# Kernel tuning notes

Hardware: AMD Instinct MI355X
Metric: run time of the kernel (lower is better)

Reference implementation:

```python
import jax, jax.numpy as jnp
import numpy as np

B, L, D, H = 2, 4096, 512, 8
HD = D // H
SCALE = 1.0 / (D / H) ** 0.5


def setup_inputs() -> dict:
    key = jax.random.key(0)
    ks = jax.random.split(key, 12)
    s = 0.02
    inp = {
        "q": jax.random.normal(ks[0], (B, L, D), jnp.float32),
        "k": jax.random.normal(ks[1], (B, L, D), jnp.float32),
        "v": jax.random.normal(ks[2], (B, L, D), jnp.float32),
        # causal mask, True = keep (masked_fill where mask == False)
        "mask": jnp.tril(jnp.ones((L, L), bool))[None, None, :, :],
        "Wq": jax.random.normal(ks[3], (D, D), jnp.float32) * s,
        "bq": jnp.zeros((D,), jnp.float32),
        "Wk": jax.random.normal(ks[4], (D, D), jnp.float32) * s,
        "bk": jnp.zeros((D,), jnp.float32),
        "Wv": jax.random.normal(ks[5], (D, D), jnp.float32) * s,
        "bv": jnp.zeros((D,), jnp.float32),
        "Wo": jax.random.normal(ks[6], (D, D), jnp.float32) * s,
        "bo": jnp.zeros((D,), jnp.float32),
    }
    return inp


def _split_heads(x):
    # [B, L, D] -> [B, H, L, HD]
    b, l, d = x.shape
    return x.reshape(b, l, H, HD).transpose(0, 2, 1, 3)


def reference(q, k, v, mask, Wq, bq, Wk, bk, Wv, bv, Wo, bo):
    # Dropout is inference-mode (identity), matching module.eval().
    qh = _split_heads(q @ Wq.T + bq)          # [B,H,L,HD]
    kh = _split_heads(k @ Wk.T + bk)          # [B,H,L,HD]
    vh = _split_heads(v @ Wv.T + bv)          # [B,H,L,HD]
    scores = jnp.einsum("bhqd,bhkd->bhqk", qh, kh) * SCALE
    scores = jnp.where(mask, scores, -jnp.inf)
    attn = jax.nn.softmax(scores, axis=-1)
    out = jnp.einsum("bhqk,bhkd->bhqd", attn, vh)  # [B,H,L,HD]
    out = out.transpose(0, 2, 1, 3).reshape(q.shape[0], q.shape[1], D)
    return out @ Wo.T + bo
```

## Files before the change

### kernel.cpp

```cpp
#include <hip/hip_runtime.h>

typedef __bf16 bf16;
typedef __bf16 bf16x4 __attribute__((ext_vector_type(4)));
typedef __bf16 bf16x8 __attribute__((ext_vector_type(8)));
typedef float  f32x4  __attribute__((ext_vector_type(4)));
typedef float  f32x16 __attribute__((ext_vector_type(16)));
typedef unsigned int u32x2 __attribute__((ext_vector_type(2)));
typedef unsigned int u32x4 __attribute__((ext_vector_type(4)));

#define NB   2
#define NL   4096
#define ND   512
#define NH   8
#define NHD  64

static __device__ __forceinline__ void g2l16(const bf16* g, bf16* l) {
    __builtin_amdgcn_global_load_lds(
        (const __attribute__((address_space(1))) unsigned int*)g,
        (__attribute__((address_space(3))) unsigned int*)l, 16, 0, 0);
}

__global__ __launch_bounds__(256) void cvt_all(
    const float* __restrict__ q, const float* __restrict__ k, const float* __restrict__ v,
    const float* __restrict__ Wq, const float* __restrict__ Wk,
    const float* __restrict__ Wv, const float* __restrict__ Wo,
    bf16* __restrict__ qb, bf16* __restrict__ kb, bf16* __restrict__ vb,
    bf16* __restrict__ wqb, bf16* __restrict__ wkb,
    bf16* __restrict__ wvb, bf16* __restrict__ wob)
{
    const int z = blockIdx.z;
    const float* src; bf16* dst; int n4;
    switch (z) {
        case 0: src = q;  dst = qb;  n4 = NB * NL * ND / 4; break;
        case 1: src = k;  dst = kb;  n4 = NB * NL * ND / 4; break;
        case 2: src = v;  dst = vb;  n4 = NB * NL * ND / 4; break;
        case 3: src = Wq; dst = wqb; n4 = ND * ND / 4; break;
        case 4: src = Wk; dst = wkb; n4 = ND * ND / 4; break;
        case 5: src = Wv; dst = wvb; n4 = ND * ND / 4; break;
        default: src = Wo; dst = wob; n4 = ND * ND / 4; break;
    }
    for (int i = blockIdx.x * 256 + threadIdx.x; i < n4; i += gridDim.x * 256) {
        const f32x4 a = *(const f32x4*)(src + (size_t)i * 4);
        bf16x4 o;
        #pragma unroll
        for (int j = 0; j < 4; ++j) o[j] = (bf16)a[j];
        *(bf16x4*)(dst + (size_t)i * 4) = o;
    }
}

__global__ __launch_bounds__(256) void proj_qkv(
    const bf16* __restrict__ qb, const bf16* __restrict__ kb, const bf16* __restrict__ vb,
    const bf16* __restrict__ wq, const bf16* __restrict__ wk, const bf16* __restrict__ wv,
    const float* __restrict__ biasq, const float* __restrict__ biask, const float* __restrict__ biasv,
    bf16* __restrict__ qh, bf16* __restrict__ kh, bf16* __restrict__ vt)
{
    const int z = blockIdx.z;
    const bf16* X     = (z == 0) ? qb : (z == 1) ? kb : vb;
    const bf16* W     = (z == 0) ? wq : (z == 1) ? wk : wv;
    const float* bias = (z == 0) ? biasq : (z == 1) ? biask : biasv;

    const int m0 = blockIdx.y * 128;
    const int n0 = blockIdx.x * 128;

    __shared__ bf16 As[2][128 * 32];
    __shared__ bf16 Bs[2][128 * 32];

    const int t    = threadIdx.x;
    const int lane = t & 63;
    const int wm   = (t >> 7) & 1;
    const int wn   = (t >> 6) & 1;
    const int quad = lane >> 4;
    const int l16  = lane & 15;

    auto stage = [&](int k0, int buf) {
        #pragma unroll
        for (int p = 0; p < 2; ++p) {
            const int id = p * 256 + t;
            const int r = id >> 2, s = id & 3;
            const int c = (s ^ (r & 3)) * 8;
            g2l16(X + (size_t)(m0 + r) * ND + k0 + c, As[buf] + id * 8);
            g2l16(W + (size_t)(n0 + r) * ND + k0 + c, Bs[buf] + id * 8);
        }
    };

    f32x4 acc[4][4] = {};
    stage(0, 0);

    for (int it = 0; it < 16; ++it) {
        __syncthreads();
        if (it + 1 < 16) stage((it + 1) * 32, (it + 1) & 1);

        const bf16* as = As[it & 1];
        const bf16* bs = Bs[it & 1];
        bf16x8 aF[4], bF[4];
        #pragma unroll
        for (int i = 0; i < 4; ++i) {
            const int ra = wm * 64 + i * 16 + l16;
            const int rb = wn * 64 + i * 16 + l16;
            aF[i] = *(const bf16x8*)(as + ra * 32 + (quad ^ (ra & 3)) * 8);
            bF[i] = *(const bf16x8*)(bs + rb * 32 + (quad ^ (rb & 3)) * 8);
        }
        #pragma unroll
        for (int mt = 0; mt < 4; ++mt)
            #pragma unroll
            for (int nt = 0; nt < 4; ++nt)
                acc[mt][nt] = __builtin_amdgcn_mfma_f32_16x16x32_bf16(
                    aF[mt], bF[nt], acc[mt][nt], 0, 0, 0);
    }

    const float oscale = (z == 0) ? 0.125f : (z == 1) ? 1.4426950408889634f : 1.0f;
    #pragma unroll
    for (int nt = 0; nt < 4; ++nt) {
        const int col = n0 + wn * 64 + nt * 16 + l16;
        const float bb = bias[col];
        const int h = col >> 6, hd = col & 63;
        #pragma unroll
        for (int mt = 0; mt < 4; ++mt) {
            const int row0 = m0 + wm * 64 + mt * 16 + quad * 4;
            const int b = row0 >> 12;
            const int l = row0 & 4095;
            if (z == 2) {
                bf16x4 val;
                #pragma unroll
                for (int r = 0; r < 4; ++r) val[r] = (bf16)(acc[mt][nt][r] + bb);
                *(bf16x4*)(vt + ((size_t)(b * NH + h) * NHD + hd) * NL + l) = val;
            } else {
                bf16* dst = (z == 0) ? qh : kh;
                #pragma unroll
                for (int r = 0; r < 4; ++r)
                    dst[((size_t)(b * NH + h) * NL + (l + r)) * NHD + hd] =
                        (bf16)((acc[mt][nt][r] + bb) * oscale);
            }
        }
    }
}

__global__ __launch_bounds__(512, 1) void attn(
    const bf16* __restrict__ qh, const bf16* __restrict__ kh,
    const bf16* __restrict__ vt, bf16* __restrict__ ao)
{
    const int bh  = blockIdx.x;
    const int b   = bh >> 3, h = bh & 7;
    const int qtA = blockIdx.y;
    const int qtB = 31 - qtA;
    const int nA  = 2 * qtA + 2;

    __shared__ bf16 smem[65536];

    const int t    = threadIdx.x;
    const int wave = t >> 6;
    const int g    = wave >> 2;
    const int w4   = wave & 3;
    const int lane = t & 63;
    const int l32  = lane & 31;
    const int half = lane >> 5;
    const int sb   = g * 32768;
    const int tg   = t & 255;
    const int qrow_l = w4 * 32 + l32;

    const bf16* Qg = qh + (size_t)bh * NL * NHD;
    const bf16* Kg = kh + (size_t)bh * NL * NHD;
    const bf16* Vg = vt + (size_t)bh * NHD * NL;

    auto kv_of = [&](int jn) -> int {
        return (g == 0) ? jn : ((jn < nA) ? jn : jn - nA + 33);
    };

    auto stage_kv = [&](int k0, int buf) {
        bf16* kd = smem + sb + buf * 8192;
        #pragma unroll
        for (int p = 0; p < 2; ++p) {
            const int id = p * 256 + tg;
            const int r = id >> 3, s = id & 7;
            g2l16(Kg + (size_t)(k0 + r) * NHD + ((s ^ (r & 7)) * 8), kd + id * 8);
            g2l16(Vg + (size_t)r * NL + k0 + ((s ^ (r & 7)) * 8), kd + 4096 + id * 8);
        }
    };

    stage_kv(kv_of(0) * 64, 0);
    stage_kv(kv_of(1) * 64, 1);
    stage_kv(kv_of(2) * 64, 2);

    bf16x8 qf[4];
    {
        const int qt0 = (g == 0) ? qtB : qtA;
        const bf16* Qt = Qg + (size_t)(qt0 * 128 + qrow_l) * NHD;
        #pragma unroll
        for (int c = 0; c < 4; ++c)
            qf[c] = *(const bf16x8*)(Qt + c * 16 + half * 8);
    }

    f32x16 o_acc[2] = {};
    float l_lane = 0.f;

    for (int jj = 0; jj < 33; ++jj) {
        if (jj < 31)       asm volatile("s_waitcnt vmcnt(8)" ::: "memory");
        else if (jj == 31) asm volatile("s_waitcnt vmcnt(4)" ::: "memory");
        else               asm volatile("s_waitcnt vmcnt(0)" ::: "memory");
        __builtin_amdgcn_sched_barrier(0);
        __builtin_amdgcn_s_barrier();
        __builtin_amdgcn_sched_barrier(0);

        if (jj + 3 < 33) stage_kv(kv_of(jj + 3) * 64, (jj + 3) & 3);

        if (g == 1 && jj == nA) {
            const float lt = l_lane + __shfl_xor(l_lane, 32, 64);
            const float rcp = 1.0f / fmaxf(lt, 1e-20f);
            const int row = qtA * 128 + qrow_l;
            #pragma unroll
            for (int mt2 = 0; mt2 < 2; ++mt2)
                #pragma unroll
                for (int rr = 0; rr < 4; ++rr) {
                    const int hd = mt2 * 32 + rr * 8 + half * 4;
                    bf16x4 val;
                    #pragma unroll
                    for (int rb = 0; rb < 4; ++rb)
                        val[rb] = (bf16)(o_acc[mt2][rr * 4 + rb] * rcp);
                    *(bf16x4*)(ao + ((size_t)b * NL + row) * ND + h * NHD + hd) = val;
                }
            o_acc[0] = (f32x16)(0.f); o_acc[1] = (f32x16)(0.f);
            l_lane = 0.f;
            const bf16* Qt = Qg + (size_t)(qtB * 128 + qrow_l) * NHD;
            #pragma unroll
            for (int c = 0; c < 4; ++c)
                qf[c] = *(const bf16x8*)(Qt + c * 16 + half * 8);
        }

        const bool useA  = (g == 1) && (jj < nA);
        const int j_glob = kv_of(jj);
        const int qt_cur = useA ? qtA : qtB;

        const bf16* ks = smem + sb + (jj & 3) * 8192;
        const bf16* vs = ks + 4096;

        f32x16 sacc[2] = {};
        #pragma unroll
        for (int c = 0; c < 4; ++c) {
            #pragma unroll
            for (int mt = 0; mt < 2; ++mt) {
                const int row   = mt * 32 + l32;
                const int chunk = 2 * c + half;
                const bf16x8 kf = *(const bf16x8*)(ks + row * 64 + ((chunk ^ (row & 7)) * 8));
                sacc[mt] = __builtin_amdgcn_mfma_f32_32x32x16_bf16(
                    kf, qf[c], sacc[mt], 0, 0, 0);
            }
        }

        const bool diag = (j_glob >= 2 * qt_cur);
        const int  dq   = j_glob * 64 - qt_cur * 128;
        #pragma unroll
        for (int mt = 0; mt < 2; ++mt) {
            #pragma unroll
            for (int r = 0; r < 16; ++r) {
                const int kv = mt * 32 + (r & 3) + 8 * (r >> 2) + 4 * half;
                float e;
                if (diag && (dq + kv > qrow_l)) e = 0.f;
                else e = __builtin_amdgcn_exp2f(sacc[mt][r]);
                l_lane += e;
                sacc[mt][r] = e;
            }
        }

        #pragma unroll
        for (int c = 0; c < 4; ++c) {
            const int mt = c >> 1;
            const int b0 = (c & 1) * 8;
            unsigned w0, w1, w2, w3;
            asm("v_cvt_pk_bf16_f32 %0, %1, %2" : "=v"(w0)
                : "v"(sacc[mt][b0 + 0]), "v"(sacc[mt][b0 + 1]));
            asm("v_cvt_pk_bf16_f32 %0, %1, %2" : "=v"(w1)
                : "v"(sacc[mt][b0 + 2]), "v"(sacc[mt][b0 + 3]));
            asm("v_cvt_pk_bf16_f32 %0, %1, %2" : "=v"(w2)
                : "v"(sacc[mt][b0 + 4]), "v"(sacc[mt][b0 + 5]));
            asm("v_cvt_pk_bf16_f32 %0, %1, %2" : "=v"(w3)
                : "v"(sacc[mt][b0 + 6]), "v"(sacc[mt][b0 + 7]));
            const u32x2 s02 = __builtin_amdgcn_permlane32_swap(w0, w2, false, false);
            const u32x2 s13 = __builtin_amdgcn_permlane32_swap(w1, w3, false, false);
            u32x4 pw_ = { s02.x, s13.x, s02.y, s13.y };
            bf16x8 pf;
            __builtin_memcpy(&pf, &pw_, 16);
            #pragma unroll
            for (int mt2 = 0; mt2 < 2; ++mt2) {
                const int row = mt2 * 32 + l32;
                const int u8  = 2 * c + half;
                const bf16x8 vf = *(const bf16x8*)(vs + row * 64 + ((u8 ^ (row & 7)) * 8));
                o_acc[mt2] = __builtin_amdgcn_mfma_f32_32x32x16_bf16(
                    vf, pf, o_acc[mt2], 0, 0, 0);
            }
        }
    }

    __syncthreads();
    float* comb = (float*)smem;
    if (g == 1) {
        const int base = w4 * (64 * 36) + lane * 36;
        #pragma unroll
        for (int mt2 = 0; mt2 < 2; ++mt2)
            #pragma unroll
            for (int i = 0; i < 16; ++i)
                comb[base + mt2 * 16 + i] = o_acc[mt2][i];
        const float lt = l_lane + __shfl_xor(l_lane, 32, 64);
        if (half == 0) comb[9216 + w4 * 32 + l32] = lt;
    }
    __syncthreads();
    if (g == 0) {
        const int base = w4 * (64 * 36) + lane * 36;
        const float lt = l_lane + __shfl_xor(l_lane, 32, 64)
                       + comb[9216 + w4 * 32 + l32];
        const float rcp = 1.0f / fmaxf(lt, 1e-20f);
        const int row = qtB * 128 + qrow_l;
        #pragma unroll
        for (int mt2 = 0; mt2 < 2; ++mt2)
            #pragma unroll
            for (int rr = 0; rr < 4; ++rr) {
                const int hd = mt2 * 32 + rr * 8 + half * 4;
                bf16x4 val;
                #pragma unroll
                for (int rb = 0; rb < 4; ++rb)
                    val[rb] = (bf16)((o_acc[mt2][rr * 4 + rb] +
                                      comb[base + mt2 * 16 + rr * 4 + rb]) * rcp);
                *(bf16x4*)(ao + ((size_t)b * NL + row) * ND + h * NHD + hd) = val;
            }
    }
}

__global__ __launch_bounds__(256) void out_proj(
    const bf16* __restrict__ ao, const bf16* __restrict__ wo,
    const float* __restrict__ bo, float* __restrict__ out)
{
    const int m0 = blockIdx.y * 128;
    const int n0 = blockIdx.x * 128;

    __shared__ bf16 As[2][128 * 32];
    __shared__ bf16 Bs[2][128 * 32];

    const int t    = threadIdx.x;
    const int lane = t & 63;
    const int wm   = (t >> 7) & 1;
    const int wn   = (t >> 6) & 1;
    const int quad = lane >> 4;
    const int l16  = lane & 15;

    auto stage = [&](int k0, int buf) {
        #pragma unroll
        for (int p = 0; p < 2; ++p) {
            const int id = p * 256 + t;
            const int r = id >> 2, s = id & 3;
            const int c = (s ^ (r & 3)) * 8;
            g2l16(ao + (size_t)(m0 + r) * ND + k0 + c, As[buf] + id * 8);
            g2l16(wo + (size_t)(n0 + r) * ND + k0 + c, Bs[buf] + id * 8);
        }
    };

    f32x4 acc[4][4] = {};
    stage(0, 0);

    for (int it = 0; it < 16; ++it) {
        __syncthreads();
        if (it + 1 < 16) stage((it + 1) * 32, (it + 1) & 1);

        const bf16* as = As[it & 1];
        const bf16* bs = Bs[it & 1];
        bf16x8 aF[4], bF[4];
        #pragma unroll
        for (int i = 0; i < 4; ++i) {
            const int ra = wm * 64 + i * 16 + l16;
            const int rb = wn * 64 + i * 16 + l16;
            aF[i] = *(const bf16x8*)(as + ra * 32 + (quad ^ (ra & 3)) * 8);
            bF[i] = *(const bf16x8*)(bs + rb * 32 + (quad ^ (rb & 3)) * 8);
        }
        #pragma unroll
        for (int mt = 0; mt < 4; ++mt)
            #pragma unroll
            for (int nt = 0; nt < 4; ++nt)
                acc[mt][nt] = __builtin_amdgcn_mfma_f32_16x16x32_bf16(
                    aF[mt], bF[nt], acc[mt][nt], 0, 0, 0);
    }

    #pragma unroll
    for (int nt = 0; nt < 4; ++nt) {
        const int col = n0 + wn * 64 + nt * 16 + l16;
        const float bb = bo[col];
        #pragma unroll
        for (int mt = 0; mt < 4; ++mt) {
            const int row0 = m0 + wm * 64 + mt * 16 + quad * 4;
            #pragma unroll
            for (int r = 0; r < 4; ++r)
                out[(size_t)(row0 + r) * ND + col] = acc[mt][nt][r] + bb;
        }
    }
}

extern "C" void kernel_launch(void* const* d_in, const int* in_sizes, int n_in,
                              void* d_out, int out_size, void* d_ws, size_t ws_size,
                              hipStream_t stream) {
    (void)in_sizes; (void)n_in; (void)out_size; (void)ws_size;

    const float* q  = (const float*)d_in[0];
    const float* k  = (const float*)d_in[1];
    const float* v  = (const float*)d_in[2];
    const float* Wq = (const float*)d_in[4];
    const float* bq = (const float*)d_in[5];
    const float* Wk = (const float*)d_in[6];
    const float* bk = (const float*)d_in[7];
    const float* Wv = (const float*)d_in[8];
    const float* bv = (const float*)d_in[9];
    const float* Wo = (const float*)d_in[10];
    const float* bo = (const float*)d_in[11];

    const size_t XSZ = (size_t)NB * NL * ND;
    const size_t WSZ = (size_t)ND * ND;
    bf16* p = (bf16*)d_ws;
    bf16* qb  = p; p += XSZ;
    bf16* kb  = p; p += XSZ;
    bf16* vb  = p; p += XSZ;
    bf16* wqb = p; p += WSZ;
    bf16* wkb = p; p += WSZ;
    bf16* wvb = p; p += WSZ;
    bf16* wob = p; p += WSZ;
    bf16* qh  = p; p += XSZ;
    bf16* kh  = p; p += XSZ;
    bf16* vt  = p; p += XSZ;
    bf16* ao  = p; p += XSZ;

    cvt_all<<<dim3(512, 1, 7), 256, 0, stream>>>(
        q, k, v, Wq, Wk, Wv, Wo, qb, kb, vb, wqb, wkb, wvb, wob);

    dim3 g1(ND / 128, (NB * NL) / 128, 3);
    proj_qkv<<<g1, 256, 0, stream>>>(qb, kb, vb, wqb, wkb, wvb, bq, bk, bv, qh, kh, vt);

    dim3 g2(16, 16, 1);
    attn<<<g2, 512, 0, stream>>>(qh, kh, vt, ao);

    dim3 g3(ND / 128, (NB * NL) / 128, 1);
    out_proj<<<g3, 256, 0, stream>>>(ao, wob, bo, (float*)d_out);
}
```

Baseline: 243.9 us.

## Load K/V tiles directly from global into registers instead of LDS staging

```diff
diff --git a/kernel.cpp b/kernel.cpp
--- a/kernel.cpp
+++ b/kernel.cpp
@@ -145,7 +145,7 @@
     const int qtB = 31 - qtA;
     const int nA  = 2 * qtA + 2;
 
-    __shared__ bf16 smem[65536];
+    __shared__ float comb[4 * 64 * 36 + 128];
 
     const int t    = threadIdx.x;
     const int wave = t >> 6;
@@ -154,8 +154,6 @@
     const int lane = t & 63;
     const int l32  = lane & 31;
     const int half = lane >> 5;
-    const int sb   = g * 32768;
-    const int tg   = t & 255;
     const int qrow_l = w4 * 32 + l32;
 
     const bf16* Qg = qh + (size_t)bh * NL * NHD;
@@ -166,20 +164,15 @@
         return (g == 0) ? jn : ((jn < nA) ? jn : jn - nA + 33);
     };
 
-    auto stage_kv = [&](int k0, int buf) {
-        bf16* kd = smem + sb + buf * 8192;
-        #pragma unroll
-        for (int p = 0; p < 2; ++p) {
-            const int id = p * 256 + tg;
-            const int r = id >> 3, s = id & 7;
-            g2l16(Kg + (size_t)(k0 + r) * NHD + ((s ^ (r & 7)) * 8), kd + id * 8);
-            g2l16(Vg + (size_t)r * NL + k0 + ((s ^ (r & 7)) * 8), kd + 4096 + id * 8);
-        }
-    };
-
-    stage_kv(kv_of(0) * 64, 0);
-    stage_kv(kv_of(1) * 64, 1);
-    stage_kv(kv_of(2) * 64, 2);
+    auto load_k = [&](int j64, bf16x8 (&kf)[8]) {
+        const int k0 = j64 * 64;
+        #pragma unroll
+        for (int c = 0; c < 4; ++c)
+            #pragma unroll
+            for (int m = 0; m < 2; ++m)
+                kf[c * 2 + m] = *(const bf16x8*)(
+                    Kg + (size_t)(k0 + m * 32 + l32) * NHD + (2 * c + half) * 8);
+    };
 
     bf16x8 qf[4];
     {
@@ -191,60 +184,58 @@
     }
 
     f32x16 o_acc[2] = {};
-    float l_lane = 0.f;
-
-    for (int jj = 0; jj < 33; ++jj) {
-        if (jj < 31)       asm volatile("s_waitcnt vmcnt(8)" ::: "memory");
-        else if (jj == 31) asm volatile("s_waitcnt vmcnt(4)" ::: "memory");
-        else               asm volatile("s_waitcnt vmcnt(0)" ::: "memory");
-        __builtin_amdgcn_sched_barrier(0);
-        __builtin_amdgcn_s_barrier();
-        __builtin_amdgcn_sched_barrier(0);
-
-        if (jj + 3 < 33) stage_kv(kv_of(jj + 3) * 64, (jj + 3) & 3);
-
-        if (g == 1 && jj == nA) {
-            const float lt = l_lane + __shfl_xor(l_lane, 32, 64);
-            const float rcp = 1.0f / fmaxf(lt, 1e-20f);
-            const int row = qtA * 128 + qrow_l;
-            #pragma unroll
-            for (int mt2 = 0; mt2 < 2; ++mt2)
+    float lacc[2] = {0.f, 0.f};
+
+    auto write_out = [&](int qt, float rcp) {
+        const int row = qt * 128 + qrow_l;
+        #pragma unroll
+        for (int mt2 = 0; mt2 < 2; ++mt2)
+            #pragma unroll
+            for (int rr = 0; rr < 4; ++rr) {
+                const int hd = mt2 * 32 + rr * 8 + half * 4;
+                bf16x4 val;
                 #pragma unroll
-                for (int rr = 0; rr < 4; ++rr) {
-                    const int hd = mt2 * 32 + rr * 8 + half * 4;
-                    bf16x4 val;
-                    #pragma unroll
-                    for (int rb = 0; rb < 4; ++rb)
-                        val[rb] = (bf16)(o_acc[mt2][rr * 4 + rb] * rcp);
-                    *(bf16x4*)(ao + ((size_t)b * NL + row) * ND + h * NHD + hd) = val;
-                }
-            o_acc[0] = (f32x16)(0.f); o_acc[1] = (f32x16)(0.f);
-            l_lane = 0.f;
-            const bf16* Qt = Qg + (size_t)(qtB * 128 + qrow_l) * NHD;
-            #pragma unroll
-            for (int c = 0; c < 4; ++c)
-                qf[c] = *(const bf16x8*)(Qt + c * 16 + half * 8);
-        }
-
+                for (int rb = 0; rb < 4; ++rb)
+                    val[rb] = (bf16)(o_acc[mt2][rr * 4 + rb] * rcp);
+                *(bf16x4*)(ao + ((size_t)b * NL + row) * ND + h * NHD + hd) = val;
+            }
+    };
+
+    auto mid_epilogue = [&]() {
+        float lt = lacc[0] + lacc[1];
+        lt += __shfl_xor(lt, 32, 64);
+        write_out(qtA, 1.0f / fmaxf(lt, 1e-20f));
+        o_acc[0] = (f32x16)(0.f); o_acc[1] = (f32x16)(0.f);
+        lacc[0] = 0.f; lacc[1] = 0.f;
+        const bf16* Qt = Qg + (size_t)(qtB * 128 + qrow_l) * NHD;
+        #pragma unroll
+        for (int c = 0; c < 4; ++c)
+            qf[c] = *(const bf16x8*)(Qt + c * 16 + half * 8);
+    };
+
+    auto do_iter = [&](int jj, const bf16x8 (&kf)[8]) {
         const bool useA  = (g == 1) && (jj < nA);
         const int j_glob = kv_of(jj);
         const int qt_cur = useA ? qtA : qtB;
-
-        const bf16* ks = smem + sb + (jj & 3) * 8192;
-        const bf16* vs = ks + 4096;
+        const int k0     = j_glob * 64;
+
+        bf16x8 vf[8];
+        #pragma unroll
+        for (int c = 0; c < 4; ++c)
+            #pragma unroll
+            for (int m = 0; m < 2; ++m)
+                vf[c * 2 + m] = *(const bf16x8*)(
+                    Vg + (size_t)(m * 32 + l32) * NL + k0 + (2 * c + half) * 8);
 
         f32x16 sacc[2] = {};
-        #pragma unroll
-        for (int c = 0; c < 4; ++c) {
-            #pragma unroll
-            for (int mt = 0; mt < 2; ++mt) {
-                const int row   = mt * 32 + l32;
-                const int chunk = 2 * c + half;
-                const bf16x8 kf = *(const bf16x8*)(ks + row * 64 + ((chunk ^ (row & 7)) * 8));
+        __builtin_amdgcn_s_setprio(1);
+        #pragma unroll
+        for (int c = 0; c < 4; ++c)
+            #pragma unroll
+            for (int mt = 0; mt < 2; ++mt)
                 sacc[mt] = __builtin_amdgcn_mfma_f32_32x32x16_bf16(
-                    kf, qf[c], sacc[mt], 0, 0, 0);
-            }
-        }
+                    kf[c * 2 + mt], qf[c], sacc[mt], 0, 0, 0);
+        __builtin_amdgcn_s_setprio(0);
 
         const bool diag = (j_glob >= 2 * qt_cur);
         const int  dq   = j_glob * 64 - qt_cur * 128;
@@ -256,7 +247,7 @@
                 float e;
                 if (diag && (dq + kv > qrow_l)) e = 0.f;
                 else e = __builtin_amdgcn_exp2f(sacc[mt][r]);
-                l_lane += e;
+                lacc[mt] += e;
                 sacc[mt][r] = e;
             }
         }
@@ -279,19 +270,31 @@
             u32x4 pw_ = { s02.x, s13.x, s02.y, s13.y };
             bf16x8 pf;
             __builtin_memcpy(&pf, &pw_, 16);
-            #pragma unroll
-            for (int mt2 = 0; mt2 < 2; ++mt2) {
-                const int row = mt2 * 32 + l32;
-                const int u8  = 2 * c + half;
-                const bf16x8 vf = *(const bf16x8*)(vs + row * 64 + ((u8 ^ (row & 7)) * 8));
+            __builtin_amdgcn_s_setprio(1);
+            #pragma unroll
+            for (int mt2 = 0; mt2 < 2; ++mt2)
                 o_acc[mt2] = __builtin_amdgcn_mfma_f32_32x32x16_bf16(
-                    vf, pf, o_acc[mt2], 0, 0, 0);
-            }
-        }
+                    vf[c * 2 + mt2], pf, o_acc[mt2], 0, 0, 0);
+            __builtin_amdgcn_s_setprio(0);
+        }
+    };
+
+    bf16x8 kA[8], kB[8];
+    load_k(kv_of(0), kA);
+
+    for (int jp = 0; jp < 17; ++jp) {
+        const int j0 = 2 * jp;
+        if (j0 + 1 < 33) load_k(kv_of(j0 + 1), kB);
+        if (g == 1 && j0 == nA) mid_epilogue();
+        do_iter(j0, kA);
+        if (j0 + 1 >= 33) break;
+        const int j1 = j0 + 1;
+        if (j1 + 1 < 33) load_k(kv_of(j1 + 1), kA);
+        if (g == 1 && j1 == nA) mid_epilogue();
+        do_iter(j1, kB);
     }
 
     __syncthreads();
-    float* comb = (float*)smem;
     if (g == 1) {
         const int base = w4 * (64 * 36) + lane * 36;
         #pragma unroll
@@ -299,14 +302,16 @@
             #pragma unroll
             for (int i = 0; i < 16; ++i)
                 comb[base + mt2 * 16 + i] = o_acc[mt2][i];
-        const float lt = l_lane + __shfl_xor(l_lane, 32, 64);
+        float lt = lacc[0] + lacc[1];
+        lt += __shfl_xor(lt, 32, 64);
         if (half == 0) comb[9216 + w4 * 32 + l32] = lt;
     }
     __syncthreads();
     if (g == 0) {
         const int base = w4 * (64 * 36) + lane * 36;
-        const float lt = l_lane + __shfl_xor(l_lane, 32, 64)
-                       + comb[9216 + w4 * 32 + l32];
+        float lt = lacc[0] + lacc[1];
+        lt += __shfl_xor(lt, 32, 64);
+        lt += comb[9216 + w4 * 32 + l32];
         const float rcp = 1.0f / fmaxf(lt, 1e-20f);
         const int row = qtB * 128 + qrow_l;
         #pragma unroll
```

Result: slower. 307.3 us (+26.0%).
